# Optimization experiments

Measured on AMD Instinct MI355X. Metric: run time of the kernel, lower is better.

The kernel has to match this reference:

```python
import jax, jax.numpy as jnp
import numpy as np

SQRT2 = 1.4142135623730951
B, C, T, J = 32, 4, 262144, 8


def _dw_corr(x, f):
    # depthwise VALID cross-correlation of (B,C,T) with 1-D filter f
    ch = x.shape[1]
    w = jnp.tile(f[None, None, :], (ch, 1, 1))  # (C,1,m)
    return jax.lax.conv_general_dilated(
        x, w, (1,), 'VALID', feature_group_count=ch,
        dimension_numbers=('NCH', 'OIH', 'NCH'))


def colfilter(x, h):
    # 'same' true convolution with odd-length filter h, zero padding
    p = h.shape[0] // 2
    xp = jnp.pad(x, ((0, 0), (0, 0), (p, p)))
    return _dw_corr(xp, jnp.flip(h))


def colifilt(x, ha, hb):
    # dtcwt synthesis upsampling filter bank (even-length qshift filters,
    # m//2 odd for 10-tap), zero extension (padding_mode='zeros').
    # Output length 2T; phase convention of dtcwt colifilt with ta=t, tb=t-1.
    b, c, t = x.shape
    m2 = ha.shape[0] // 2  # 5 for 10-tap qshift
    xp = jnp.pad(x, ((0, 0), (0, 0), (m2, m2)))  # length t+10
    L = t // 2 + 4
    seq_b = xp[:, :, 1::2][:, :, :L]      # padded indices 1,3,...,t+7
    seq_a = xp[:, :, 0::2][:, :, 1:L + 1]  # padded indices 2,4,...,t+8
    hao, hae = jnp.flip(ha[0::2]), jnp.flip(ha[1::2])  # odd/even taps of tree-a filter
    hbo, hbe = jnp.flip(hb[0::2]), jnp.flip(hb[1::2])
    y0 = _dw_corr(seq_b, hao)  # output samples 4s
    y1 = _dw_corr(seq_a, hbo)  # 4s+1
    y2 = _dw_corr(seq_b, hae)  # 4s+2
    y3 = _dw_corr(seq_a, hbe)  # 4s+3
    return jnp.stack([y0, y1, y2, y3], axis=-1).reshape(b, c, 2 * t)


def c2q(bp_r, bp_i, scale):
    # complex -> real: real part to even samples, imag part to odd samples
    b, c, th = bp_r.shape
    return (jnp.stack([bp_r, bp_i], axis=-1) * scale).reshape(b, c, 2 * th)


def inv_j2plus(lo, bp_r, bp_i, g0a, g1a, g0b, g1b):
    # one coarse synthesis level: interleave complex bandpass, then
    hi = c2q(bp_r, bp_i, SQRT2)
    return colifilt(lo, g0b, g0a) + colifilt(hi, g1b, g1a)


def inv_j1(lo, bp_r, bp_i, g0o, g1o):
    # finest synthesis level: full-rate biorthogonal filters, no upsampling
    hi = c2q(bp_r, bp_i, SQRT2)
    return colfilter(lo, g0o) + colfilter(hi, g1o)


def setup_inputs():
    key = jax.random.key(0)
    ks = jax.random.split(key, 32)
    inp = {}
    inp['yl'] = jax.random.normal(ks[0], (B, C, T // 2 ** (J - 1)), jnp.float32)
    for j in range(J):
        tj = T // 2 ** (j + 1)
        inp[f'yh{j}_r'] = jax.random.normal(ks[2 * j + 1], (B, C, tj), jnp.float32)
        inp[f'yh{j}_i'] = jax.random.normal(ks[2 * j + 2], (B, C, tj), jnp.float32)

    def filt(k, n):
        f = jax.random.normal(k, (n,), jnp.float32)
        return f / jnp.linalg.norm(f)

    inp['g0o'] = filt(ks[20], 7)   # near_sym_a synthesis lowpass (7-tap)
    inp['g1o'] = filt(ks[21], 5)   # near_sym_a synthesis highpass (5-tap)
    g0a = filt(ks[22], 10)         # qshift_a 10-tap
    g1a = filt(ks[23], 10)
    inp['g0a'], inp['g0b'] = g0a, jnp.flip(g0a)  # tree-b = time-reversed tree-a
    inp['g1a'], inp['g1b'] = g1a, jnp.flip(g1a)
    return inp


def reference(yl, yh0_r, yh0_i, yh1_r, yh1_i, yh2_r, yh2_i, yh3_r, yh3_i,
              yh4_r, yh4_i, yh5_r, yh5_i, yh6_r, yh6_i, yh7_r, yh7_i,
              g0o, g1o, g0a, g0b, g1a, g1b):
    yh = [(yh0_r, yh0_i), (yh1_r, yh1_i), (yh2_r, yh2_i), (yh3_r, yh3_i),
          (yh4_r, yh4_i), (yh5_r, yh5_i), (yh6_r, yh6_i), (yh7_r, yh7_i)]
    x = yl
    for j in range(J - 1, 0, -1):  # coarse-to-fine, doubles length each level
        x = inv_j2plus(x, yh[j][0], yh[j][1], g0a, g1a, g0b, g1b)
    return inv_j1(x, yh[0][0], yh[0][1], g0o, g1o)
```

## Files before the change

### kernel.cpp

```cpp
#include <hip/hip_runtime.h>

#define PBLOCK 256
#define FBLOCK 128
#define FT 512

typedef float v2f __attribute__((ext_vector_type(2)));

static __device__ __forceinline__ float ldz(const float* __restrict__ p, int i, int n) {
    return (i >= 0 && i < n) ? p[i] : 0.f;
}

#define BAR_LGKM() do { \
    asm volatile("s_waitcnt lgkmcnt(0)" ::: "memory"); \
    __builtin_amdgcn_s_barrier(); \
} while (0)

#define BAR_FULL() do { \
    asm volatile("s_waitcnt vmcnt(0) lgkmcnt(0)" ::: "memory"); \
    __builtin_amdgcn_s_barrier(); \
} while (0)

#define AS1C(p) ((const __attribute__((address_space(1))) unsigned int*)(p))
#define AS3(p)  ((__attribute__((address_space(3))) unsigned int*)(p))

struct QFilt {
    float b0e[5], b0o[5], a0e[5], a0o[5];
    float b1e[5], b1o[5], a1e[5], a1o[5];
};

static __device__ __forceinline__ QFilt load_qfilt(
    const float* __restrict__ g0a, const float* __restrict__ g0b,
    const float* __restrict__ g1a, const float* __restrict__ g1b) {
    const float S2 = 1.4142135623730951f;
    QFilt f;
#pragma unroll
    for (int i = 0; i < 5; ++i) {
        f.b0e[i] = g0b[8 - 2 * i]; f.b0o[i] = g0b[9 - 2 * i];
        f.a0e[i] = g0a[8 - 2 * i]; f.a0o[i] = g0a[9 - 2 * i];
        f.b1e[i] = S2 * g1b[8 - 2 * i]; f.b1o[i] = S2 * g1b[9 - 2 * i];
        f.a1e[i] = S2 * g1a[8 - 2 * i]; f.a1o[i] = S2 * g1a[9 - 2 * i];
    }
    return f;
}

struct QFiltP {
    v2f f01l[5], f23l[5], f01h[5], f23h[5];
};

static __device__ __forceinline__ QFiltP load_qfiltp(
    const float* __restrict__ g0a, const float* __restrict__ g0b,
    const float* __restrict__ g1a, const float* __restrict__ g1b) {
    const float S2 = 1.4142135623730951f;
    QFiltP f;
#pragma unroll
    for (int i = 0; i < 5; ++i) {
        float b0e = g0b[8 - 2 * i], b0o = g0b[9 - 2 * i];
        float a0e = g0a[8 - 2 * i], a0o = g0a[9 - 2 * i];
        float b1e = S2 * g1b[8 - 2 * i], b1o = S2 * g1b[9 - 2 * i];
        float a1e = S2 * g1a[8 - 2 * i], a1o = S2 * g1a[9 - 2 * i];
        f.f01l[i] = (v2f){b0e, a0e};
        f.f23l[i] = (v2f){b0o, a0o};
        f.f01h[i] = (v2f){b1e, a1e};
        f.f23h[i] = (v2f){b1o, a1o};
    }
    return f;
}

static __device__ __forceinline__ float4 quad_p(
    const float* base, int loOff, int riOff, int ioff, const QFiltP& f) {
    v2f y01 = (v2f){0.f, 0.f}, y23 = (v2f){0.f, 0.f};
#pragma unroll
    for (int i = 0; i < 5; ++i) {
        v2f lo2 = *reinterpret_cast<const v2f*>(base + loOff + 2 * i);
        v2f ri;
        ri.x = base[riOff + i];
        ri.y = base[riOff + ioff + i];
        y01 = __builtin_elementwise_fma(lo2, f.f01l[i], y01);
        y23 = __builtin_elementwise_fma(lo2, f.f23l[i], y23);
        y01 = __builtin_elementwise_fma(ri, f.f01h[i], y01);
        y23 = __builtin_elementwise_fma(ri, f.f23h[i], y23);
    }
    return make_float4(y01.x, y01.y, y23.x, y23.y);
}

static __device__ __forceinline__ float4 quad_i(
    const float* __restrict__ lo_s, int lobase,
    const float* __restrict__ r_s, const float* __restrict__ i_s, int ribase,
    const QFilt& f) {
    float y0 = 0.f, y1 = 0.f, y2 = 0.f, y3 = 0.f;
#pragma unroll
    for (int i = 0; i < 5; ++i) {
        float ve = lo_s[lobase + 2 * i], vo = lo_s[lobase + 2 * i + 1];
        float vr = r_s[ribase + i], vi = i_s[ribase + i];
        y0 = fmaf(ve, f.b0e[i], y0); y2 = fmaf(ve, f.b0o[i], y2);
        y1 = fmaf(vo, f.a0e[i], y1); y3 = fmaf(vo, f.a0o[i], y3);
        y0 = fmaf(vr, f.b1e[i], y0); y2 = fmaf(vr, f.b1o[i], y2);
        y1 = fmaf(vi, f.a1e[i], y1); y3 = fmaf(vi, f.a1o[i], y3);
    }
    return make_float4(y0, y1, y2, y3);
}

static __device__ __forceinline__ float4 quad_d(
    const float* __restrict__ Ae, const float* __restrict__ Ao, int base,
    const float* __restrict__ r_s, const float* __restrict__ i_s, int ribase,
    const QFilt& f) {
    float y0 = 0.f, y1 = 0.f, y2 = 0.f, y3 = 0.f;
#pragma unroll
    for (int i = 0; i < 5; ++i) {
        float ve = Ae[base + i], vo = Ao[base + i];
        float vr = r_s[ribase + i], vi = i_s[ribase + i];
        y0 = fmaf(ve, f.b0e[i], y0); y2 = fmaf(ve, f.b0o[i], y2);
        y1 = fmaf(vo, f.a0e[i], y1); y3 = fmaf(vo, f.a0o[i], y3);
        y0 = fmaf(vr, f.b1e[i], y0); y2 = fmaf(vr, f.b1o[i], y2);
        y1 = fmaf(vi, f.a1e[i], y1); y3 = fmaf(vi, f.a1o[i], y3);
    }
    return make_float4(y0, y1, y2, y3);
}

__global__ void __launch_bounds__(PBLOCK) pair_lvl(
    const float* __restrict__ up,
    const float* __restrict__ ru, const float* __restrict__ iu,
    const float* __restrict__ rl, const float* __restrict__ il,
    float* __restrict__ out,
    const float* __restrict__ g0a, const float* __restrict__ g0b,
    const float* __restrict__ g1a, const float* __restrict__ g1b,
    int L)
{
    __shared__ __align__(16) float upw[272], ruw[140], iuw[140], rlw[264], ilw[264];
    __shared__ __align__(16) float Ae[260], Ao[260];
    int tid = threadIdx.x, bx = blockIdx.x, row = blockIdx.y;
    int lup = L >> 2, lu8 = L >> 3, lql = L >> 2;
    const float* uprow = up + (size_t)row * lup;
    const float* rurow = ru + (size_t)row * lu8;
    const float* iurow = iu + (size_t)row * lu8;
    const float* rlrow = rl + (size_t)row * lql;
    const float* ilrow = il + (size_t)row * lql;
    bool bnd = (bx == 0) || (bx == (int)gridDim.x - 1);
    int S = bx << 8;
    int sAu = (S >> 1) - 1;
    int gu = S - 8;
    int gru = (S >> 1) - 4;
    int grl = S - 4;

    for (int i = tid; i < 270; i += PBLOCK) {
        const float* src; float* dst; int k, gb, len;
        if (i < 68)       { src = uprow; dst = upw; k = i;       gb = gu + 4 * k;  len = lup; }
        else if (i < 103) { src = rurow; dst = ruw; k = i - 68;  gb = gru + 4 * k; len = lu8; }
        else if (i < 138) { src = iurow; dst = iuw; k = i - 103; gb = gru + 4 * k; len = lu8; }
        else if (i < 204) { src = rlrow; dst = rlw; k = i - 138; gb = grl + 4 * k; len = lql; }
        else              { src = ilrow; dst = ilw; k = i - 204; gb = grl + 4 * k; len = lql; }
        float4 v;
        if (!bnd) v = *reinterpret_cast<const float4*>(src + gb);
        else { v.x = ldz(src, gb, len); v.y = ldz(src, gb + 1, len);
               v.z = ldz(src, gb + 2, len); v.w = ldz(src, gb + 3, len); }
        *reinterpret_cast<float4*>(dst + 4 * k) = v;
    }
    __syncthreads();

    QFilt f = load_qfilt(g0a, g0b, g1a, g1b);
    if (tid < 130) {
        float4 q = quad_i(upw, 2 * tid + 2, ruw, iuw, tid + 1, f);
        if (bnd) {
            int sp = sAu + tid;
            if (sp < 0 || sp >= lu8) q = make_float4(0.f, 0.f, 0.f, 0.f);
        }
        Ae[2 * tid] = q.x; Ae[2 * tid + 1] = q.z;
        Ao[2 * tid] = q.y; Ao[2 * tid + 1] = q.w;
    }
    __syncthreads();

    float4 res = quad_d(Ae, Ao, tid, rlw, ilw, tid + 2, f);
    reinterpret_cast<float4*>(out + (size_t)row * L)[S + tid] = res;
}

#define O_X4 0
#define O_R3 80
#define O_I3 120
#define O_R2 160
#define O_I2 232
#define O_R1 304
#define O_I1 440
#define O_X3 576
#define O_X2 720
#define O_X1 992
#define W_TOT 1512
#define NSLOT 144

static __device__ __forceinline__ void slot_map(
    int i, int v0, int u0, int s0, int t4, int t8, int t16,
    const float* x4row, const float* r3row, const float* i3row,
    const float* r2row, const float* i2row,
    const float* r1row, const float* i1row,
    const float*& src, int& gb, int& len)
{
    if (i < 20)       { src = x4row; int k = i;       gb = 2 * v0 - 8 + 4 * k; len = t8;  }
    else if (i < 30)  { src = r3row; int k = i - 20;  gb = v0 - 4 + 4 * k;     len = t16; }
    else if (i < 40)  { src = i3row; int k = i - 30;  gb = v0 - 4 + 4 * k;     len = t16; }
    else if (i < 58)  { src = r2row; int k = i - 40;  gb = u0 - 4 + 4 * k;     len = t8;  }
    else if (i < 76)  { src = i2row; int k = i - 58;  gb = u0 - 4 + 4 * k;     len = t8;  }
    else if (i < 110) { src = r1row; int k = i - 76;  gb = s0 - 4 + 4 * k;     len = t4;  }
    else              { src = i1row; int k = i - 110; gb = s0 - 4 + 4 * k;     len = t4;  }
}

__global__ void __launch_bounds__(FBLOCK) final4_async(
    const float* __restrict__ x4,
    const float* __restrict__ r3, const float* __restrict__ i3,
    const float* __restrict__ r2, const float* __restrict__ i2,
    const float* __restrict__ r1, const float* __restrict__ i1,
    const float* __restrict__ r0, const float* __restrict__ i0,
    float* __restrict__ out,
    const float* __restrict__ g0a, const float* __restrict__ g0b,
    const float* __restrict__ g1a, const float* __restrict__ g1b,
    const float* __restrict__ g0o, const float* __restrict__ g1o,
    int T_)
{
    const float S2 = 1.4142135623730951f;
    __shared__ __align__(16) float W[W_TOT];

    int row = blockIdx.y, tid = threadIdx.x, bx = blockIdx.x;
    int t2 = T_ >> 1, t4 = T_ >> 2, t8 = T_ >> 3, t16 = T_ >> 4;
    int s0 = bx << 7, u0 = bx << 6, v0 = bx << 5, h0 = bx << 8;
    const float* x4row = x4 + (size_t)row * t8;
    const float* r3row = r3 + (size_t)row * t16;
    const float* i3row = i3 + (size_t)row * t16;
    const float* r2row = r2 + (size_t)row * t8;
    const float* i2row = i2 + (size_t)row * t8;
    const float* r1row = r1 + (size_t)row * t4;
    const float* i1row = i1 + (size_t)row * t4;
    const float* r0row = r0 + (size_t)row * t2;
    const float* i0row = i0 + (size_t)row * t2;
    bool bnd = (bx == 0) || (bx == (int)gridDim.x - 1);

    if (!bnd) {
        {
            const float* src; int gb, len;
            slot_map(tid, v0, u0, s0, t4, t8, t16,
                     x4row, r3row, i3row, r2row, i2row, r1row, i1row, src, gb, len);
            __builtin_amdgcn_global_load_lds(AS1C(src + gb), AS3(W + 4 * tid), 16, 0, 0);
        }
        if (tid < NSLOT - FBLOCK) {
            const float* src; int gb, len;
            slot_map(tid + FBLOCK, v0, u0, s0, t4, t8, t16,
                     x4row, r3row, i3row, r2row, i2row, r1row, i1row, src, gb, len);
            __builtin_amdgcn_global_load_lds(AS1C(src + gb), AS3(W + 4 * (tid + FBLOCK)), 16, 0, 0);
        }
    } else {
#pragma unroll
        for (int it = 0; it < 2; ++it) {
            int i = tid + FBLOCK * it;
            if (i < NSLOT) {
                const float* src; int gb, len;
                slot_map(i, v0, u0, s0, t4, t8, t16,
                         x4row, r3row, i3row, r2row, i2row, r1row, i1row, src, gb, len);
                float4 v;
                v.x = ldz(src, gb, len);     v.y = ldz(src, gb + 1, len);
                v.z = ldz(src, gb + 2, len); v.w = ldz(src, gb + 3, len);
                *reinterpret_cast<float4*>(W + 4 * i) = v;
            }
        }
    }
    BAR_FULL();

    float rA[4], iA[4];
    {
        int u0e = h0 + 2 * tid - 1;
        if (!bnd) {
            float4 va = *reinterpret_cast<const float4*>(r0row + u0e);
            float4 vb = *reinterpret_cast<const float4*>(i0row + u0e);
            rA[0] = va.x; rA[1] = va.y; rA[2] = va.z; rA[3] = va.w;
            iA[0] = vb.x; iA[1] = vb.y; iA[2] = vb.z; iA[3] = vb.w;
        } else {
#pragma unroll
            for (int e = 0; e < 4; ++e) {
                rA[e] = ldz(r0row, u0e + e, t2);
                iA[e] = ldz(i0row, u0e + e, t2);
            }
        }
    }

    QFiltP f = load_qfiltp(g0a, g0b, g1a, g1b);
    float g0r[7], g1r[5];
#pragma unroll
    for (int j = 0; j < 7; ++j) g0r[j] = g0o[j];
#pragma unroll
    for (int j = 0; j < 5; ++j) g1r[j] = S2 * g1o[j];

    if (tid < 36) {
        int k = tid;
        float4 q = quad_p(W, O_X4 + 2 * k, O_R3 + k, 40, f);
        if (bnd) {
            int v = v0 - 2 + k;
            if (v < 0 || v >= t16) q = make_float4(0.f, 0.f, 0.f, 0.f);
        }
        *reinterpret_cast<float4*>(W + O_X3 + 4 * k) = q;
    }
    BAR_LGKM();

    if (tid < 68) {
        int k = tid;
        float4 q = quad_p(W, O_X3 + 2 * k, O_R2 + k, 72, f);
        if (bnd) {
            int u = u0 - 2 + k;
            if (u < 0 || u >= t8) q = make_float4(0.f, 0.f, 0.f, 0.f);
        }
        *reinterpret_cast<float4*>(W + O_X2 + 4 * k) = q;
    }
    BAR_LGKM();

    float4 myq;
    {
        int l = tid;
        float4 q = quad_p(W, O_X2 + 2 * l + 2, O_R1 + l + 1, 136, f);
        if (bnd) {
            int s = s0 - 1 + l;
            if (s < 0 || s >= t4) q = make_float4(0.f, 0.f, 0.f, 0.f);
        }
        myq = q;
        *reinterpret_cast<float4*>(W + O_X1 + 4 * l) = q;
        if (tid < 2) {
            int l2 = FBLOCK + tid;
            q = quad_p(W, O_X2 + 2 * l2 + 2, O_R1 + l2 + 1, 136, f);
            if (bnd) {
                int s = s0 - 1 + l2;
                if (s < 0 || s >= t4) q = make_float4(0.f, 0.f, 0.f, 0.f);
            }
            *reinterpret_cast<float4*>(W + O_X1 + 4 * l2) = q;
        }
    }
    BAR_LGKM();

    float w[12];
    *reinterpret_cast<float4*>(&w[0]) = myq;
    *reinterpret_cast<float4*>(&w[4]) = *reinterpret_cast<const float4*>(W + O_X1 + 4 * (tid + 1));
    *reinterpret_cast<float4*>(&w[8]) = *reinterpret_cast<const float4*>(W + O_X1 + 4 * (tid + 2));

    float o[4];
#pragma unroll
    for (int p = 0; p < 4; ++p) {
        float acc = 0.f;
#pragma unroll
        for (int j = 0; j < 7; ++j)
            acc = fmaf(g0r[j], w[p + 7 - j], acc);
#pragma unroll
        for (int j = 0; j < 5; ++j) {
            int e = p + 4 - j;
            float v = (e & 1) ? iA[e >> 1] : rA[e >> 1];
            acc = fmaf(g1r[j], v, acc);
        }
        o[p] = acc;
    }
    reinterpret_cast<float4*>(out + (size_t)row * T_)[s0 + tid] =
        make_float4(o[0], o[1], o[2], o[3]);
}

extern "C" void kernel_launch(void* const* d_in, const int* in_sizes, int n_in,
                              void* d_out, int out_size, void* d_ws, size_t ws_size,
                              hipStream_t stream)
{
    const float* yl = (const float*)d_in[0];
    const float* yhr[8]; const float* yhi[8];
    for (int j = 0; j < 8; ++j) {
        yhr[j] = (const float*)d_in[1 + 2 * j];
        yhi[j] = (const float*)d_in[2 + 2 * j];
    }
    const float* g0o = (const float*)d_in[17];
    const float* g1o = (const float*)d_in[18];
    const float* g0a = (const float*)d_in[19];
    const float* g0b = (const float*)d_in[20];
    const float* g1a = (const float*)d_in[21];
    const float* g1b = (const float*)d_in[22];

    const int BC = 32 * 4;
    const int T_ = 262144;

    float* x4buf = (float*)d_ws;
    float* x6buf = (float*)((char*)d_ws + ((size_t)32 << 20));

    {
        dim3 grid(8192 / 1024, BC);
        pair_lvl<<<grid, PBLOCK, 0, stream>>>(
            yl, yhr[7], yhi[7], yhr[6], yhi[6], x6buf,
            g0a, g0b, g1a, g1b, 8192);
    }
    {
        dim3 grid(32768 / 1024, BC);
        pair_lvl<<<grid, PBLOCK, 0, stream>>>(
            x6buf, yhr[5], yhi[5], yhr[4], yhi[4], x4buf,
            g0a, g0b, g1a, g1b, 32768);
    }
    dim3 grid(T_ / FT, BC);
    final4_async<<<grid, FBLOCK, 0, stream>>>(
        x4buf, yhr[3], yhi[3], yhr[2], yhi[2], yhr[1], yhi[1],
        yhr[0], yhi[0], (float*)d_out,
        g0a, g0b, g1a, g1b, g0o, g1o, T_);
}
```

Measured before the change: 106.9 us.

## Make final kernel persistent over 8 tiles with double-buffered async LDS staging

The final fused kernel now processes eight consecutive tiles per block instead of one. While the current tile is computed, it prefetches the next tile's inputs into a second LDS buffer via global_load_lds, and also prefetches the next epilogue registers. Partial vmcnt waits let the current tile start while the next tile's loads are still in flight. This hides global-load latency and amortizes filter setup, but cuts the grid size by eight, raises LDS use, and depends on hand-counted vmcnt values being correct.

```diff
diff --git a/kernel.cpp b/kernel.cpp
--- a/kernel.cpp
+++ b/kernel.cpp
@@ -3,6 +3,7 @@
 #define PBLOCK 256
 #define FBLOCK 128
 #define FT 512
+#define TPB 8
 
 typedef float v2f __attribute__((ext_vector_type(2)));
 
@@ -12,11 +13,6 @@
 
 #define BAR_LGKM() do { \
     asm volatile("s_waitcnt lgkmcnt(0)" ::: "memory"); \
-    __builtin_amdgcn_s_barrier(); \
-} while (0)
-
-#define BAR_FULL() do { \
-    asm volatile("s_waitcnt vmcnt(0) lgkmcnt(0)" ::: "memory"); \
     __builtin_amdgcn_s_barrier(); \
 } while (0)
 
@@ -180,10 +176,11 @@
 #define O_I2 232
 #define O_R1 304
 #define O_I1 440
-#define O_X3 576
-#define O_X2 720
-#define O_X1 992
-#define W_TOT 1512
+#define SBUF 576
+#define O_X3 1152
+#define O_X2 1296
+#define O_X1 1568
+#define W_TOT 2088
 #define NSLOT 144
 
 static __device__ __forceinline__ void slot_map(
@@ -202,7 +199,7 @@
     else              { src = i1row; int k = i - 110; gb = s0 - 4 + 4 * k;     len = t4;  }
 }
 
-__global__ void __launch_bounds__(FBLOCK) final4_async(
+__global__ void __launch_bounds__(FBLOCK) final4_db(
     const float* __restrict__ x4,
     const float* __restrict__ r3, const float* __restrict__ i3,
     const float* __restrict__ r2, const float* __restrict__ i2,
@@ -218,8 +215,9 @@
     __shared__ __align__(16) float W[W_TOT];
 
     int row = blockIdx.y, tid = threadIdx.x, bx = blockIdx.x;
+    int lane = tid & 63, wv = tid >> 6;
     int t2 = T_ >> 1, t4 = T_ >> 2, t8 = T_ >> 3, t16 = T_ >> 4;
-    int s0 = bx << 7, u0 = bx << 6, v0 = bx << 5, h0 = bx << 8;
+    int NT = T_ >> 9;
     const float* x4row = x4 + (size_t)row * t8;
     const float* r3row = r3 + (size_t)row * t16;
     const float* i3row = i3 + (size_t)row * t16;
@@ -229,22 +227,35 @@
     const float* i1row = i1 + (size_t)row * t4;
     const float* r0row = r0 + (size_t)row * t2;
     const float* i0row = i0 + (size_t)row * t2;
-    bool bnd = (bx == 0) || (bx == (int)gridDim.x - 1);
-
-    if (!bnd) {
+
+    QFiltP f = load_qfiltp(g0a, g0b, g1a, g1b);
+    float g0r[7], g1r[5];
+#pragma unroll
+    for (int j = 0; j < 7; ++j) g0r[j] = g0o[j];
+#pragma unroll
+    for (int j = 0; j < 5; ++j) g1r[j] = S2 * g1o[j];
+
+    int tile0 = bx * TPB;
+
+    auto stage_async = [&](int tile, int sb) {
+        int v0 = tile << 5, u0 = tile << 6, s0 = tile << 7;
         {
+            int slot = wv * 72 + lane;
             const float* src; int gb, len;
-            slot_map(tid, v0, u0, s0, t4, t8, t16,
+            slot_map(slot, v0, u0, s0, t4, t8, t16,
                      x4row, r3row, i3row, r2row, i2row, r1row, i1row, src, gb, len);
-            __builtin_amdgcn_global_load_lds(AS1C(src + gb), AS3(W + 4 * tid), 16, 0, 0);
-        }
-        if (tid < NSLOT - FBLOCK) {
+            __builtin_amdgcn_global_load_lds(AS1C(src + gb), AS3(W + sb + 4 * slot), 16, 0, 0);
+        }
+        if (lane < 8) {
+            int slot = wv * 72 + 64 + lane;
             const float* src; int gb, len;
-            slot_map(tid + FBLOCK, v0, u0, s0, t4, t8, t16,
+            slot_map(slot, v0, u0, s0, t4, t8, t16,
                      x4row, r3row, i3row, r2row, i2row, r1row, i1row, src, gb, len);
-            __builtin_amdgcn_global_load_lds(AS1C(src + gb), AS3(W + 4 * (tid + FBLOCK)), 16, 0, 0);
-        }
-    } else {
+            __builtin_amdgcn_global_load_lds(AS1C(src + gb), AS3(W + sb + 4 * slot), 16, 0, 0);
+        }
+    };
+    auto stage_reg = [&](int tile, int sb) {
+        int v0 = tile << 5, u0 = tile << 6, s0 = tile << 7;
 #pragma unroll
         for (int it = 0; it < 2; ++it) {
             int i = tid + FBLOCK * it;
@@ -255,102 +266,130 @@
                 float4 v;
                 v.x = ldz(src, gb, len);     v.y = ldz(src, gb + 1, len);
                 v.z = ldz(src, gb + 2, len); v.w = ldz(src, gb + 3, len);
-                *reinterpret_cast<float4*>(W + 4 * i) = v;
-            }
-        }
-    }
-    BAR_FULL();
-
-    float rA[4], iA[4];
+                *reinterpret_cast<float4*>(W + sb + 4 * i) = v;
+            }
+        }
+    };
+    auto load_epi = [&](int tile, bool bnd, float4& pr, float4& pi) {
+        int u0e = (tile << 8) + 2 * tid - 1;
+        if (!bnd) {
+            pr = *reinterpret_cast<const float4*>(r0row + u0e);
+            pi = *reinterpret_cast<const float4*>(i0row + u0e);
+        } else {
+            pr.x = ldz(r0row, u0e, t2);     pr.y = ldz(r0row, u0e + 1, t2);
+            pr.z = ldz(r0row, u0e + 2, t2); pr.w = ldz(r0row, u0e + 3, t2);
+            pi.x = ldz(i0row, u0e, t2);     pi.y = ldz(i0row, u0e + 1, t2);
+            pi.z = ldz(i0row, u0e + 2, t2); pi.w = ldz(i0row, u0e + 3, t2);
+        }
+    };
+
+    float4 prc, pic, prn, pin;
     {
-        int u0e = h0 + 2 * tid - 1;
-        if (!bnd) {
-            float4 va = *reinterpret_cast<const float4*>(r0row + u0e);
-            float4 vb = *reinterpret_cast<const float4*>(i0row + u0e);
-            rA[0] = va.x; rA[1] = va.y; rA[2] = va.z; rA[3] = va.w;
-            iA[0] = vb.x; iA[1] = vb.y; iA[2] = vb.z; iA[3] = vb.w;
+        bool b0 = (tile0 == 0) || (tile0 == NT - 1);
+        if (!b0) stage_async(tile0, 0); else stage_reg(tile0, 0);
+        load_epi(tile0, b0, prc, pic);
+    }
+
+    int cur = 0;
+    for (int t = 0; t < TPB; ++t) {
+        int tile = tile0 + t;
+        bool bndc = (tile == 0) || (tile == NT - 1);
+        int s0 = tile << 7, u0 = tile << 6, v0 = tile << 5;
+        int SB = cur * SBUF;
+
+        if (t + 1 < TPB) {
+            int ntile = tile + 1;
+            bool bndn = (ntile == NT - 1);
+            if (!bndn) {
+                stage_async(ntile, (cur ^ 1) * SBUF);
+                load_epi(ntile, false, prn, pin);
+                if (t == 0) { asm volatile("s_waitcnt vmcnt(4) lgkmcnt(0)" ::: "memory"); }
+                else        { asm volatile("s_waitcnt vmcnt(5) lgkmcnt(0)" ::: "memory"); }
+                __builtin_amdgcn_s_barrier();
+            } else {
+                stage_reg(ntile, (cur ^ 1) * SBUF);
+                load_epi(ntile, true, prn, pin);
+                asm volatile("s_waitcnt vmcnt(0) lgkmcnt(0)" ::: "memory");
+                __builtin_amdgcn_s_barrier();
+            }
         } else {
-#pragma unroll
-            for (int e = 0; e < 4; ++e) {
-                rA[e] = ldz(r0row, u0e + e, t2);
-                iA[e] = ldz(i0row, u0e + e, t2);
-            }
-        }
-    }
-
-    QFiltP f = load_qfiltp(g0a, g0b, g1a, g1b);
-    float g0r[7], g1r[5];
-#pragma unroll
-    for (int j = 0; j < 7; ++j) g0r[j] = g0o[j];
-#pragma unroll
-    for (int j = 0; j < 5; ++j) g1r[j] = S2 * g1o[j];
-
-    if (tid < 36) {
-        int k = tid;
-        float4 q = quad_p(W, O_X4 + 2 * k, O_R3 + k, 40, f);
-        if (bnd) {
-            int v = v0 - 2 + k;
-            if (v < 0 || v >= t16) q = make_float4(0.f, 0.f, 0.f, 0.f);
-        }
-        *reinterpret_cast<float4*>(W + O_X3 + 4 * k) = q;
-    }
-    BAR_LGKM();
-
-    if (tid < 68) {
-        int k = tid;
-        float4 q = quad_p(W, O_X3 + 2 * k, O_R2 + k, 72, f);
-        if (bnd) {
-            int u = u0 - 2 + k;
-            if (u < 0 || u >= t8) q = make_float4(0.f, 0.f, 0.f, 0.f);
-        }
-        *reinterpret_cast<float4*>(W + O_X2 + 4 * k) = q;
-    }
-    BAR_LGKM();
-
-    float4 myq;
-    {
-        int l = tid;
-        float4 q = quad_p(W, O_X2 + 2 * l + 2, O_R1 + l + 1, 136, f);
-        if (bnd) {
-            int s = s0 - 1 + l;
-            if (s < 0 || s >= t4) q = make_float4(0.f, 0.f, 0.f, 0.f);
-        }
-        myq = q;
-        *reinterpret_cast<float4*>(W + O_X1 + 4 * l) = q;
-        if (tid < 2) {
-            int l2 = FBLOCK + tid;
-            q = quad_p(W, O_X2 + 2 * l2 + 2, O_R1 + l2 + 1, 136, f);
-            if (bnd) {
-                int s = s0 - 1 + l2;
+            asm volatile("s_waitcnt vmcnt(0) lgkmcnt(0)" ::: "memory");
+            __builtin_amdgcn_s_barrier();
+        }
+
+        if (tid < 36) {
+            int k = tid;
+            float4 q = quad_p(W, SB + O_X4 + 2 * k, SB + O_R3 + k, 40, f);
+            if (bndc) {
+                int v = v0 - 2 + k;
+                if (v < 0 || v >= t16) q = make_float4(0.f, 0.f, 0.f, 0.f);
+            }
+            *reinterpret_cast<float4*>(W + O_X3 + 4 * k) = q;
+        }
+        BAR_LGKM();
+
+        if (tid < 68) {
+            int k = tid;
+            float4 q = quad_p(W, O_X3 + 2 * k, SB + O_R2 + k, 72, f);
+            if (bndc) {
+                int u = u0 - 2 + k;
+                if (u < 0 || u >= t8) q = make_float4(0.f, 0.f, 0.f, 0.f);
+            }
+            *reinterpret_cast<float4*>(W + O_X2 + 4 * k) = q;
+        }
+        BAR_LGKM();
+
+        float4 myq;
+        {
+            int l = tid;
+            float4 q = quad_p(W, O_X2 + 2 * l + 2, SB + O_R1 + l + 1, 136, f);
+            if (bndc) {
+                int s = s0 - 1 + l;
                 if (s < 0 || s >= t4) q = make_float4(0.f, 0.f, 0.f, 0.f);
             }
-            *reinterpret_cast<float4*>(W + O_X1 + 4 * l2) = q;
-        }
-    }
-    BAR_LGKM();
-
-    float w[12];
-    *reinterpret_cast<float4*>(&w[0]) = myq;
-    *reinterpret_cast<float4*>(&w[4]) = *reinterpret_cast<const float4*>(W + O_X1 + 4 * (tid + 1));
-    *reinterpret_cast<float4*>(&w[8]) = *reinterpret_cast<const float4*>(W + O_X1 + 4 * (tid + 2));
-
-    float o[4];
-#pragma unroll
-    for (int p = 0; p < 4; ++p) {
-        float acc = 0.f;
-#pragma unroll
-        for (int j = 0; j < 7; ++j)
-            acc = fmaf(g0r[j], w[p + 7 - j], acc);
-#pragma unroll
-        for (int j = 0; j < 5; ++j) {
-            int e = p + 4 - j;
-            float v = (e & 1) ? iA[e >> 1] : rA[e >> 1];
-            acc = fmaf(g1r[j], v, acc);
-        }
-        o[p] = acc;
-    }
-    reinterpret_cast<float4*>(out + (size_t)row * T_)[s0 + tid] =
-        make_float4(o[0], o[1], o[2], o[3]);
+            myq = q;
+            *reinterpret_cast<float4*>(W + O_X1 + 4 * l) = q;
+            if (tid < 2) {
+                int l2 = FBLOCK + tid;
+                q = quad_p(W, O_X2 + 2 * l2 + 2, SB + O_R1 + l2 + 1, 136, f);
+                if (bndc) {
+                    int s = s0 - 1 + l2;
+                    if (s < 0 || s >= t4) q = make_float4(0.f, 0.f, 0.f, 0.f);
+                }
+                *reinterpret_cast<float4*>(W + O_X1 + 4 * l2) = q;
+            }
+        }
+        BAR_LGKM();
+
+        float w[12];
+        *reinterpret_cast<float4*>(&w[0]) = myq;
+        *reinterpret_cast<float4*>(&w[4]) = *reinterpret_cast<const float4*>(W + O_X1 + 4 * (tid + 1));
+        *reinterpret_cast<float4*>(&w[8]) = *reinterpret_cast<const float4*>(W + O_X1 + 4 * (tid + 2));
+
+        float rAv[4] = { prc.x, prc.y, prc.z, prc.w };
+        float iAv[4] = { pic.x, pic.y, pic.z, pic.w };
+
+        float o[4];
+#pragma unroll
+        for (int p = 0; p < 4; ++p) {
+            float acc = 0.f;
+#pragma unroll
+            for (int j = 0; j < 7; ++j)
+                acc = fmaf(g0r[j], w[p + 7 - j], acc);
+#pragma unroll
+            for (int j = 0; j < 5; ++j) {
+                int e = p + 4 - j;
+                float v = (e & 1) ? iAv[e >> 1] : rAv[e >> 1];
+                acc = fmaf(g1r[j], v, acc);
+            }
+            o[p] = acc;
+        }
+        reinterpret_cast<float4*>(out + (size_t)row * T_)[s0 + tid] =
+            make_float4(o[0], o[1], o[2], o[3]);
+
+        cur ^= 1;
+        prc = prn; pic = pin;
+    }
 }
 
 extern "C" void kernel_launch(void* const* d_in, const int* in_sizes, int n_in,
@@ -388,8 +427,8 @@
             x6buf, yhr[5], yhi[5], yhr[4], yhi[4], x4buf,
             g0a, g0b, g1a, g1b, 32768);
     }
-    dim3 grid(T_ / FT, BC);
-    final4_async<<<grid, FBLOCK, 0, stream>>>(
+    dim3 grid((T_ / FT) / TPB, BC);
+    final4_db<<<grid, FBLOCK, 0, stream>>>(
         x4buf, yhr[3], yhi[3], yhr[2], yhi[2], yhr[1], yhi[1],
         yhr[0], yhi[0], (float*)d_out,
         g0a, g0b, g1a, g1b, g0o, g1o, T_);
```

After: 144.8 us. 35.5% more time.
